# Kernel optimization log

Measured on AMD Instinct MI355X. Metric: run time of the kernel, lower is better.

Reference implementation:

```python
import jax, jax.numpy as jnp
import numpy as np
from jax import lax

B, T, V, E, H = 4096, 80, 10000, 100, 64


def setup_inputs() -> dict:
    key = jax.random.key(0)
    ks = jax.random.split(key, 8)
    return {
        "tokens": jax.random.randint(ks[0], (B, T), 0, V, dtype=jnp.int32),
        "emb": jax.random.normal(ks[1], (V, E), jnp.float32) * 0.05,
        "Wx0": jax.random.normal(ks[2], (E, H), jnp.float32) * (1.0 / np.sqrt(E)),
        "Wh0": jax.random.normal(ks[3], (H, H), jnp.float32) * (1.0 / np.sqrt(H)),
        "b0": jnp.zeros((H,), jnp.float32),
        "Wx1": jax.random.normal(ks[4], (H, H), jnp.float32) * (1.0 / np.sqrt(H)),
        "Wh1": jax.random.normal(ks[5], (H, H), jnp.float32) * (1.0 / np.sqrt(H)),
        "b1": jnp.zeros((H,), jnp.float32),
        "Wout": jax.random.normal(ks[6], (H, 1), jnp.float32) * (1.0 / np.sqrt(H)),
        "bout": jnp.zeros((1,), jnp.float32),
    }


def reference(tokens, emb, Wx0, Wh0, b0, Wx1, Wh1, b1, Wout, bout):
    # Embedding lookup: [B, T, E]
    x = emb[tokens]
    batch = x.shape[0]
    h0 = jnp.zeros((batch, Wh0.shape[0]), x.dtype)
    h1 = jnp.zeros((batch, Wh1.shape[0]), x.dtype)

    def step(carry, xt):
        h0, h1 = carry
        # SimpleRNNCell: h = tanh(x @ Wx + h_prev @ Wh + b)  (dropout off in eval)
        h0 = jnp.tanh(xt @ Wx0 + h0 @ Wh0 + b0)
        h1 = jnp.tanh(h0 @ Wx1 + h1 @ Wh1 + b1)
        return (h0, h1), None

    # scan over time: xs has shape [T, B, E]
    (h0, h1), _ = lax.scan(step, (h0, h1), jnp.swapaxes(x, 0, 1))
    logits = h1 @ Wout + bout  # [B, 1]
    return jax.nn.sigmoid(logits)
```

## Files before the change

### kernel.cpp

```cpp
#include <hip/hip_runtime.h>

#define BB 4096
#define TT 80
#define VV 10000
#define EE 100
#define HH 64
#define STR 68

typedef _Float16 f16x8 __attribute__((ext_vector_type(8)));
typedef _Float16 f16x4 __attribute__((ext_vector_type(4)));
typedef __attribute__((ext_vector_type(4))) float f4v;

#define MFMA(w, s, c) __builtin_amdgcn_mfma_f32_16x16x32_f16((w), (s), (c), 0, 0, 0)

#define BAR() do { asm volatile("s_waitcnt lgkmcnt(0)" ::: "memory"); \
                   __builtin_amdgcn_s_barrier();                      \
                   asm volatile("" ::: "memory"); } while (0)

__device__ __forceinline__ float fast_tanh(float x) {
    float e = __builtin_amdgcn_exp2f(x * 2.8853900817779268f);
    return 1.0f - 2.0f * __builtin_amdgcn_rcpf(e + 1.0f);
}

__device__ __forceinline__ void load_wfrag(const float* __restrict__ W, int kf, int g,
                                           int c, f16x8& hi, f16x8& lo) {
    union { _Float16 h[8]; f16x8 v; } th, tl;
#pragma unroll
    for (int i = 0; i < 8; ++i) {
        float wv = W[(32 * kf + 8 * g + i) * HH + c];
        _Float16 hf = (_Float16)wv;
        th.h[i] = hf;
        tl.h[i] = (_Float16)(wv - (float)hf);
    }
    hi = th.v;
    lo = tl.v;
}

__global__ __launch_bounds__(256) void emb2_kernel(const float* __restrict__ emb,
                                                   const float* __restrict__ Wx0,
                                                   const float* __restrict__ b0,
                                                   _Float16* __restrict__ emb2h) {
    const int tid = threadIdx.x;
    const int wid = tid >> 6;
    const int l = tid & 63;
    const int g = l >> 4;
    const int r16 = l & 15;
    const int c = 16 * wid + r16;
    const int jcol = 16 * wid + 4 * g;
    const int vr = blockIdx.x * 16 + r16;

    f16x8 wa[4];
#pragma unroll
    for (int kf = 0; kf < 4; ++kf) {
        union { _Float16 h[8]; f16x8 v; } t;
#pragma unroll
        for (int i = 0; i < 8; ++i) {
            int e = 32 * kf + 8 * g + i;
            t.h[i] = (e < EE) ? (_Float16)Wx0[e * HH + c] : (_Float16)0.f;
        }
        wa[kf] = t.v;
    }
    const float* er = emb + (size_t)vr * EE;
    f4v acc = *(const f4v*)&b0[jcol];
#pragma unroll
    for (int kf = 0; kf < 4; ++kf) {
        union { _Float16 h[8]; f16x8 v; } tb;
#pragma unroll
        for (int i = 0; i < 8; ++i) {
            int e = 32 * kf + 8 * g + i;
            tb.h[i] = (e < EE) ? (_Float16)er[e] : (_Float16)0.f;
        }
        acc = MFMA(wa[kf], tb.v, acc);
    }
    f16x4 o;
#pragma unroll
    for (int q = 0; q < 4; ++q) o[q] = (_Float16)acc[q];
    *(f16x4*)&emb2h[(size_t)vr * HH + jcol] = o;
}

__global__ __launch_bounds__(512, 1) void rnn_pipe(
    const int* __restrict__ tokens, const _Float16* __restrict__ emb2,
    const float* __restrict__ Wh0, const float* __restrict__ Wx1,
    const float* __restrict__ Wh1, const float* __restrict__ b1,
    const float* __restrict__ Wout, const float* __restrict__ bout,
    float* __restrict__ out) {
    __shared__ __align__(16) _Float16 H0[2][16][STR];
    __shared__ __align__(16) _Float16 H1[2][16][STR];
    __shared__ __align__(16) int tokT[TT][16];
    __shared__ float Pred[4][16];

    const int tid = threadIdx.x;
    const int w8 = tid >> 6;
    const int l = tid & 63;
    const int g = l >> 4;
    const int r16 = l & 15;
    const bool isL0 = (w8 < 4);
    const int tile = isL0 ? w8 : (w8 - 4);
    const int c = 16 * tile + r16;
    const int jcol = 16 * tile + 4 * g;
    const int R = blockIdx.x * 16;

    for (int i = tid; i < 16 * TT; i += 512) {
        int r = i / TT, t = i - r * TT;
        tokT[t][r] = tokens[R * TT + i] << 7;
    }

    f16x8 wAh[2], wAl[2], wBh[2], wBl[2];
    if (isL0) {
        load_wfrag(Wh0, 0, g, c, wAh[0], wAl[0]);
        load_wfrag(Wh0, 1, g, c, wAh[1], wAl[1]);
        wBh[0] = wBh[1] = wBl[0] = wBl[1] = (f16x8)0;
    } else {
        load_wfrag(Wx1, 0, g, c, wAh[0], wAl[0]);
        load_wfrag(Wx1, 1, g, c, wAh[1], wAl[1]);
        load_wfrag(Wh1, 0, g, c, wBh[0], wBl[0]);
        load_wfrag(Wh1, 1, g, c, wBh[1], wBl[1]);
    }
    const f4v b1v = *(const f4v*)&b1[jcol];
    const f4v wov = *(const f4v*)&Wout[jcol];
    const f4v z4 = {0.f, 0.f, 0.f, 0.f};
    const char* ebase = (const char*)emb2 + (size_t)jcol * 2;

    BAR();

    f16x8 a0[2] = {(f16x8)0, (f16x8)0};
    f16x8 a1[2] = {(f16x8)0, (f16x8)0};

    f16x4 xc = (f16x4)0, xn = (f16x4)0;
    if (isL0) {
        int tb0 = tokT[0][r16];
        int tb1 = tokT[1][r16];
        xc = *(const f16x4*)(ebase + tb0);
        xn = *(const f16x4*)(ebase + tb1);
        f16x4 ph;
#pragma unroll
        for (int q = 0; q < 4; ++q) ph[q] = (_Float16)fast_tanh((float)xc[q]);
        *(f16x4*)&H0[0][r16][jcol] = ph;
        xc = xn;
    }
    BAR();
    a0[0] = *(const f16x8*)&H0[0][r16][8 * g];
    a0[1] = *(const f16x8*)&H0[0][r16][32 + 8 * g];

#pragma unroll 2
    for (int p = 1; p <= TT - 1; ++p) {
        const int par = p & 1;
        if (isL0) {
            int pn = (p + 1 <= TT - 1) ? p + 1 : TT - 1;
            int tb = tokT[pn][r16];
            xn = *(const f16x4*)(ebase + tb);
            f4v A1 = {(float)xc[0], (float)xc[1], (float)xc[2], (float)xc[3]};
            A1 = MFMA(wAh[0], a0[0], A1);
            A1 = MFMA(wAh[1], a0[1], A1);
            f4v A2 = MFMA(wAl[0], a0[0], z4);
            A2 = MFMA(wAl[1], a0[1], A2);
            f4v acc0 = A1 + A2;
            f16x4 p0;
#pragma unroll
            for (int q = 0; q < 4; ++q) p0[q] = (_Float16)fast_tanh(acc0[q]);
            *(f16x4*)&H0[par][r16][jcol] = p0;
            xc = xn;
        } else {
            f4v C1 = b1v;
            C1 = MFMA(wAh[0], a0[0], C1);
            C1 = MFMA(wAh[1], a0[1], C1);
            f4v C2 = MFMA(wAl[0], a0[0], z4);
            C2 = MFMA(wAl[1], a0[1], C2);
            f4v C3 = MFMA(wBh[0], a1[0], z4);
            C3 = MFMA(wBh[1], a1[1], C3);
            f4v C4 = MFMA(wBl[0], a1[0], z4);
            C4 = MFMA(wBl[1], a1[1], C4);
            f4v acc1 = (C1 + C2) + (C3 + C4);
            f16x4 p1;
#pragma unroll
            for (int q = 0; q < 4; ++q) p1[q] = (_Float16)fast_tanh(acc1[q]);
            *(f16x4*)&H1[par][r16][jcol] = p1;
        }
        BAR();
        a0[0] = *(const f16x8*)&H0[par][r16][8 * g];
        a0[1] = *(const f16x8*)&H0[par][r16][32 + 8 * g];
        if (!isL0) {
            a1[0] = *(const f16x8*)&H1[par][r16][8 * g];
            a1[1] = *(const f16x8*)&H1[par][r16][32 + 8 * g];
        }
    }

    if (!isL0) {
        f4v C1 = b1v;
        C1 = MFMA(wAh[0], a0[0], C1);
        C1 = MFMA(wAh[1], a0[1], C1);
        f4v C2 = MFMA(wAl[0], a0[0], z4);
        C2 = MFMA(wAl[1], a0[1], C2);
        f4v C3 = MFMA(wBh[0], a1[0], z4);
        C3 = MFMA(wBh[1], a1[1], C3);
        f4v C4 = MFMA(wBl[0], a1[0], z4);
        C4 = MFMA(wBl[1], a1[1], C4);
        f4v acc1 = (C1 + C2) + (C3 + C4);
        float pp = fast_tanh(acc1[0]) * wov[0];
        pp = fmaf(fast_tanh(acc1[1]), wov[1], pp);
        pp = fmaf(fast_tanh(acc1[2]), wov[2], pp);
        pp = fmaf(fast_tanh(acc1[3]), wov[3], pp);
        pp += __shfl_xor(pp, 16, 64);
        pp += __shfl_xor(pp, 32, 64);
        if (l < 16) Pred[tile][l] = pp;
    }
    BAR();
    if (tid < 16) {
        float logit = Pred[0][tid] + Pred[1][tid] + Pred[2][tid] +
                      Pred[3][tid] + bout[0];
        out[R + tid] = __builtin_amdgcn_rcpf(
            1.0f + __builtin_amdgcn_exp2f(-1.4426950408889634f * logit));
    }
}

extern "C" void kernel_launch(void* const* d_in, const int* in_sizes, int n_in,
                              void* d_out, int out_size, void* d_ws, size_t ws_size,
                              hipStream_t stream) {
    const int*   tokens = (const int*)  d_in[0];
    const float* emb    = (const float*)d_in[1];
    const float* Wx0    = (const float*)d_in[2];
    const float* Wh0    = (const float*)d_in[3];
    const float* b0     = (const float*)d_in[4];
    const float* Wx1    = (const float*)d_in[5];
    const float* Wh1    = (const float*)d_in[6];
    const float* b1     = (const float*)d_in[7];
    const float* Wout   = (const float*)d_in[8];
    const float* bout   = (const float*)d_in[9];
    float* out  = (float*)d_out;
    _Float16* emb2h = (_Float16*)d_ws;

    emb2_kernel<<<VV / 16, 256, 0, stream>>>(emb, Wx0, b0, emb2h);
    rnn_pipe<<<BB / 16, 512, 0, stream>>>(tokens, emb2h, Wh0, Wx1, Wh1, b1,
                                          Wout, bout, out);
}
```

Baseline: 40.89 us.

## Split layer-1 RNN work into separate input and recurrent wave roles

Result: slower. 42.59 us (+4.2%).

```diff
diff --git a/kernel.cpp b/kernel.cpp
--- a/kernel.cpp
+++ b/kernel.cpp
@@ -6,6 +6,7 @@
 #define EE 100
 #define HH 64
 #define STR 68
+#define STRP 68
 
 typedef _Float16 f16x8 __attribute__((ext_vector_type(8)));
 typedef _Float16 f16x4 __attribute__((ext_vector_type(4)));
@@ -78,7 +79,7 @@
     *(f16x4*)&emb2h[(size_t)vr * HH + jcol] = o;
 }
 
-__global__ __launch_bounds__(512, 1) void rnn_pipe(
+__global__ __launch_bounds__(768, 1) void rnn_pipe(
     const int* __restrict__ tokens, const _Float16* __restrict__ emb2,
     const float* __restrict__ Wh0, const float* __restrict__ Wx1,
     const float* __restrict__ Wh1, const float* __restrict__ b1,
@@ -86,36 +87,30 @@
     float* __restrict__ out) {
     __shared__ __align__(16) _Float16 H0[2][16][STR];
     __shared__ __align__(16) _Float16 H1[2][16][STR];
+    __shared__ __align__(16) float PP[2][16][STRP];
     __shared__ __align__(16) int tokT[TT][16];
     __shared__ float Pred[4][16];
 
     const int tid = threadIdx.x;
-    const int w8 = tid >> 6;
+    const int w12 = tid >> 6;
     const int l = tid & 63;
     const int g = l >> 4;
     const int r16 = l & 15;
-    const bool isL0 = (w8 < 4);
-    const int tile = isL0 ? w8 : (w8 - 4);
+    const int role = w12 >> 2;
+    const int tile = w12 & 3;
     const int c = 16 * tile + r16;
     const int jcol = 16 * tile + 4 * g;
     const int R = blockIdx.x * 16;
 
-    for (int i = tid; i < 16 * TT; i += 512) {
+    for (int i = tid; i < 16 * TT; i += 768) {
         int r = i / TT, t = i - r * TT;
         tokT[t][r] = tokens[R * TT + i] << 7;
     }
 
-    f16x8 wAh[2], wAl[2], wBh[2], wBl[2];
-    if (isL0) {
-        load_wfrag(Wh0, 0, g, c, wAh[0], wAl[0]);
-        load_wfrag(Wh0, 1, g, c, wAh[1], wAl[1]);
-        wBh[0] = wBh[1] = wBl[0] = wBl[1] = (f16x8)0;
-    } else {
-        load_wfrag(Wx1, 0, g, c, wAh[0], wAl[0]);
-        load_wfrag(Wx1, 1, g, c, wAh[1], wAl[1]);
-        load_wfrag(Wh1, 0, g, c, wBh[0], wBl[0]);
-        load_wfrag(Wh1, 1, g, c, wBh[1], wBl[1]);
-    }
+    const float* Wsel = (role == 0) ? Wh0 : (role == 1 ? Wx1 : Wh1);
+    f16x8 wAh[2], wAl[2];
+    load_wfrag(Wsel, 0, g, c, wAh[0], wAl[0]);
+    load_wfrag(Wsel, 1, g, c, wAh[1], wAl[1]);
     const f4v b1v = *(const f4v*)&b1[jcol];
     const f4v wov = *(const f4v*)&Wout[jcol];
     const f4v z4 = {0.f, 0.f, 0.f, 0.f};
@@ -123,15 +118,12 @@
 
     BAR();
 
-    f16x8 a0[2] = {(f16x8)0, (f16x8)0};
-    f16x8 a1[2] = {(f16x8)0, (f16x8)0};
-
+    f16x8 as0 = (f16x8)0, as1 = (f16x8)0;
     f16x4 xc = (f16x4)0, xn = (f16x4)0;
-    if (isL0) {
-        int tb0 = tokT[0][r16];
-        int tb1 = tokT[1][r16];
-        xc = *(const f16x4*)(ebase + tb0);
-        xn = *(const f16x4*)(ebase + tb1);
+
+    if (role == 0) {
+        xc = *(const f16x4*)(ebase + tokT[0][r16]);
+        xn = *(const f16x4*)(ebase + tokT[1][r16]);
         f16x4 ph;
 #pragma unroll
         for (int q = 0; q < 4; ++q) ph[q] = (_Float16)fast_tanh((float)xc[q]);
@@ -139,67 +131,77 @@
         xc = xn;
     }
     BAR();
-    a0[0] = *(const f16x8*)&H0[0][r16][8 * g];
-    a0[1] = *(const f16x8*)&H0[0][r16][32 + 8 * g];
+    if (role != 2) {
+        as0 = *(const f16x8*)&H0[0][r16][8 * g];
+        as1 = *(const f16x8*)&H0[0][r16][32 + 8 * g];
+    }
 
 #pragma unroll 2
-    for (int p = 1; p <= TT - 1; ++p) {
-        const int par = p & 1;
-        if (isL0) {
-            int pn = (p + 1 <= TT - 1) ? p + 1 : TT - 1;
-            int tb = tokT[pn][r16];
-            xn = *(const f16x4*)(ebase + tb);
-            f4v A1 = {(float)xc[0], (float)xc[1], (float)xc[2], (float)xc[3]};
-            A1 = MFMA(wAh[0], a0[0], A1);
-            A1 = MFMA(wAh[1], a0[1], A1);
-            f4v A2 = MFMA(wAl[0], a0[0], z4);
-            A2 = MFMA(wAl[1], a0[1], A2);
-            f4v acc0 = A1 + A2;
-            f16x4 p0;
-#pragma unroll
-            for (int q = 0; q < 4; ++q) p0[q] = (_Float16)fast_tanh(acc0[q]);
-            *(f16x4*)&H0[par][r16][jcol] = p0;
-            xc = xn;
+    for (int q = 1; q <= 80; ++q) {
+        const int par = q & 1;
+        if (role == 0) {
+            if (q <= TT - 1) {
+                int pn = (q + 1 <= TT - 1) ? q + 1 : TT - 1;
+                xn = *(const f16x4*)(ebase + tokT[pn][r16]);
+                f4v C1 = {(float)xc[0], (float)xc[1], (float)xc[2], (float)xc[3]};
+                C1 = MFMA(wAh[0], as0, C1);
+                C1 = MFMA(wAh[1], as1, C1);
+                f4v C2 = MFMA(wAl[0], as0, z4);
+                C2 = MFMA(wAl[1], as1, C2);
+                f4v acc = C1 + C2;
+                f16x4 ph;
+#pragma unroll
+                for (int u = 0; u < 4; ++u) ph[u] = (_Float16)fast_tanh(acc[u]);
+                *(f16x4*)&H0[par][r16][jcol] = ph;
+                xc = xn;
+            }
+        } else if (role == 1) {
+            f4v C1 = b1v;
+            C1 = MFMA(wAh[0], as0, C1);
+            C1 = MFMA(wAh[1], as1, C1);
+            f4v C2 = MFMA(wAl[0], as0, z4);
+            C2 = MFMA(wAl[1], as1, C2);
+            f4v P = C1 + C2;
+            *(f4v*)&PP[par][r16][jcol] = P;
         } else {
-            f4v C1 = b1v;
-            C1 = MFMA(wAh[0], a0[0], C1);
-            C1 = MFMA(wAh[1], a0[1], C1);
-            f4v C2 = MFMA(wAl[0], a0[0], z4);
-            C2 = MFMA(wAl[1], a0[1], C2);
-            f4v C3 = MFMA(wBh[0], a1[0], z4);
-            C3 = MFMA(wBh[1], a1[1], C3);
-            f4v C4 = MFMA(wBl[0], a1[0], z4);
-            C4 = MFMA(wBl[1], a1[1], C4);
-            f4v acc1 = (C1 + C2) + (C3 + C4);
-            f16x4 p1;
-#pragma unroll
-            for (int q = 0; q < 4; ++q) p1[q] = (_Float16)fast_tanh(acc1[q]);
-            *(f16x4*)&H1[par][r16][jcol] = p1;
+            if (q >= 2) {
+                f4v C1 = *(const f4v*)&PP[par ^ 1][r16][jcol];
+                C1 = MFMA(wAh[0], as0, C1);
+                C1 = MFMA(wAh[1], as1, C1);
+                f4v C2 = MFMA(wAl[0], as0, z4);
+                C2 = MFMA(wAl[1], as1, C2);
+                f4v acc = C1 + C2;
+                f16x4 ph;
+#pragma unroll
+                for (int u = 0; u < 4; ++u) ph[u] = (_Float16)fast_tanh(acc[u]);
+                *(f16x4*)&H1[par][r16][jcol] = ph;
+            }
         }
         BAR();
-        a0[0] = *(const f16x8*)&H0[par][r16][8 * g];
-        a0[1] = *(const f16x8*)&H0[par][r16][32 + 8 * g];
-        if (!isL0) {
-            a1[0] = *(const f16x8*)&H1[par][r16][8 * g];
-            a1[1] = *(const f16x8*)&H1[par][r16][32 + 8 * g];
-        }
-    }
-
-    if (!isL0) {
-        f4v C1 = b1v;
-        C1 = MFMA(wAh[0], a0[0], C1);
-        C1 = MFMA(wAh[1], a0[1], C1);
-        f4v C2 = MFMA(wAl[0], a0[0], z4);
-        C2 = MFMA(wAl[1], a0[1], C2);
-        f4v C3 = MFMA(wBh[0], a1[0], z4);
-        C3 = MFMA(wBh[1], a1[1], C3);
-        f4v C4 = MFMA(wBl[0], a1[0], z4);
-        C4 = MFMA(wBl[1], a1[1], C4);
-        f4v acc1 = (C1 + C2) + (C3 + C4);
-        float pp = fast_tanh(acc1[0]) * wov[0];
-        pp = fmaf(fast_tanh(acc1[1]), wov[1], pp);
-        pp = fmaf(fast_tanh(acc1[2]), wov[2], pp);
-        pp = fmaf(fast_tanh(acc1[3]), wov[3], pp);
+        if (role != 2) {
+            if (q <= TT - 1) {
+                as0 = *(const f16x8*)&H0[par][r16][8 * g];
+                as1 = *(const f16x8*)&H0[par][r16][32 + 8 * g];
+            }
+        } else {
+            if (q >= 2) {
+                as0 = *(const f16x8*)&H1[par][r16][8 * g];
+                as1 = *(const f16x8*)&H1[par][r16][32 + 8 * g];
+            }
+        }
+    }
+
+    if (role == 2) {
+        f4v C1 = *(const f4v*)&PP[0][r16][jcol];
+        C1 = MFMA(wAh[0], as0, C1);
+        C1 = MFMA(wAh[1], as1, C1);
+        f4v C2 = MFMA(wAl[0], as0, z4);
+        C2 = MFMA(wAl[1], as1, C2);
+        f4v acc = C1 + C2;
+        float pp = fast_tanh(acc[0]) * wov[0];
+        pp = fmaf(fast_tanh(acc[1]), wov[1], pp);
+        pp = fmaf(fast_tanh(acc[2]), wov[2], pp);
+        pp = fmaf(fast_tanh(acc[3]), wov[3], pp);
         pp += __shfl_xor(pp, 16, 64);
         pp += __shfl_xor(pp, 32, 64);
         if (l < 16) Pred[tile][l] = pp;
@@ -230,6 +232,6 @@
     _Float16* emb2h = (_Float16*)d_ws;
 
     emb2_kernel<<<VV / 16, 256, 0, stream>>>(emb, Wx0, b0, emb2h);
-    rnn_pipe<<<BB / 16, 512, 0, stream>>>(tokens, emb2h, Wh0, Wx1, Wh1, b1,
+    rnn_pipe<<<BB / 16, 768, 0, stream>>>(tokens, emb2h, Wh0, Wx1, Wh1, b1,
                                           Wout, bout, out);
 }
```

## Move layer-1 input projection onto layer-0 waves via shared-memory handoff

Applied to the files above, without the earlier changes.

Result: slower. 54.02 us (+32.1%).

```diff
diff --git a/kernel.cpp b/kernel.cpp
--- a/kernel.cpp
+++ b/kernel.cpp
@@ -6,6 +6,7 @@
 #define EE 100
 #define HH 64
 #define STR 68
+#define STRP 68
 
 typedef _Float16 f16x8 __attribute__((ext_vector_type(8)));
 typedef _Float16 f16x4 __attribute__((ext_vector_type(4)));
@@ -86,6 +87,7 @@
     float* __restrict__ out) {
     __shared__ __align__(16) _Float16 H0[2][16][STR];
     __shared__ __align__(16) _Float16 H1[2][16][STR];
+    __shared__ __align__(16) float PP[2][16][STRP];
     __shared__ __align__(16) int tokT[TT][16];
     __shared__ float Pred[4][16];
 
@@ -109,12 +111,12 @@
     if (isL0) {
         load_wfrag(Wh0, 0, g, c, wAh[0], wAl[0]);
         load_wfrag(Wh0, 1, g, c, wAh[1], wAl[1]);
+        load_wfrag(Wx1, 0, g, c, wBh[0], wBl[0]);
+        load_wfrag(Wx1, 1, g, c, wBh[1], wBl[1]);
+    } else {
+        load_wfrag(Wh1, 0, g, c, wAh[0], wAl[0]);
+        load_wfrag(Wh1, 1, g, c, wAh[1], wAl[1]);
         wBh[0] = wBh[1] = wBl[0] = wBl[1] = (f16x8)0;
-    } else {
-        load_wfrag(Wx1, 0, g, c, wAh[0], wAl[0]);
-        load_wfrag(Wx1, 1, g, c, wAh[1], wAl[1]);
-        load_wfrag(Wh1, 0, g, c, wBh[0], wBl[0]);
-        load_wfrag(Wh1, 1, g, c, wBh[1], wBl[1]);
     }
     const f4v b1v = *(const f4v*)&b1[jcol];
     const f4v wov = *(const f4v*)&Wout[jcol];
@@ -124,14 +126,12 @@
     BAR();
 
     f16x8 a0[2] = {(f16x8)0, (f16x8)0};
-    f16x8 a1[2] = {(f16x8)0, (f16x8)0};
-
+    f4v Pin = z4;
     f16x4 xc = (f16x4)0, xn = (f16x4)0;
+
     if (isL0) {
-        int tb0 = tokT[0][r16];
-        int tb1 = tokT[1][r16];
-        xc = *(const f16x4*)(ebase + tb0);
-        xn = *(const f16x4*)(ebase + tb1);
+        xc = *(const f16x4*)(ebase + tokT[0][r16]);
+        xn = *(const f16x4*)(ebase + tokT[1][r16]);
         f16x4 ph;
 #pragma unroll
         for (int q = 0; q < 4; ++q) ph[q] = (_Float16)fast_tanh((float)xc[q]);
@@ -139,63 +139,72 @@
         xc = xn;
     }
     BAR();
-    a0[0] = *(const f16x8*)&H0[0][r16][8 * g];
-    a0[1] = *(const f16x8*)&H0[0][r16][32 + 8 * g];
+    if (isL0) {
+        a0[0] = *(const f16x8*)&H0[0][r16][8 * g];
+        a0[1] = *(const f16x8*)&H0[0][r16][32 + 8 * g];
+    }
 
 #pragma unroll 2
-    for (int p = 1; p <= TT - 1; ++p) {
+    for (int p = 1; p <= 80; ++p) {
         const int par = p & 1;
         if (isL0) {
-            int pn = (p + 1 <= TT - 1) ? p + 1 : TT - 1;
-            int tb = tokT[pn][r16];
-            xn = *(const f16x4*)(ebase + tb);
-            f4v A1 = {(float)xc[0], (float)xc[1], (float)xc[2], (float)xc[3]};
-            A1 = MFMA(wAh[0], a0[0], A1);
-            A1 = MFMA(wAh[1], a0[1], A1);
-            f4v A2 = MFMA(wAl[0], a0[0], z4);
-            A2 = MFMA(wAl[1], a0[1], A2);
-            f4v acc0 = A1 + A2;
-            f16x4 p0;
-#pragma unroll
-            for (int q = 0; q < 4; ++q) p0[q] = (_Float16)fast_tanh(acc0[q]);
-            *(f16x4*)&H0[par][r16][jcol] = p0;
-            xc = xn;
+            if (p <= TT - 1) {
+                if (p <= TT - 2)
+                    xn = *(const f16x4*)(ebase + tokT[p + 1][r16]);
+                f4v A1 = {(float)xc[0], (float)xc[1], (float)xc[2], (float)xc[3]};
+                A1 = MFMA(wAh[0], a0[0], A1);
+                A1 = MFMA(wAh[1], a0[1], A1);
+                f4v A2 = MFMA(wAl[0], a0[0], z4);
+                A2 = MFMA(wAl[1], a0[1], A2);
+                f4v acc0 = A1 + A2;
+                f16x4 p0;
+#pragma unroll
+                for (int q = 0; q < 4; ++q) p0[q] = (_Float16)fast_tanh(acc0[q]);
+                *(f16x4*)&H0[par][r16][jcol] = p0;
+                xc = xn;
+            }
+            f4v C1 = b1v;
+            C1 = MFMA(wBh[0], a0[0], C1);
+            C1 = MFMA(wBh[1], a0[1], C1);
+            f4v C2 = MFMA(wBl[0], a0[0], z4);
+            C2 = MFMA(wBl[1], a0[1], C2);
+            *(f4v*)&PP[par][r16][jcol] = C1 + C2;
         } else {
-            f4v C1 = b1v;
-            C1 = MFMA(wAh[0], a0[0], C1);
-            C1 = MFMA(wAh[1], a0[1], C1);
-            f4v C2 = MFMA(wAl[0], a0[0], z4);
-            C2 = MFMA(wAl[1], a0[1], C2);
-            f4v C3 = MFMA(wBh[0], a1[0], z4);
-            C3 = MFMA(wBh[1], a1[1], C3);
-            f4v C4 = MFMA(wBl[0], a1[0], z4);
-            C4 = MFMA(wBl[1], a1[1], C4);
-            f4v acc1 = (C1 + C2) + (C3 + C4);
-            f16x4 p1;
-#pragma unroll
-            for (int q = 0; q < 4; ++q) p1[q] = (_Float16)fast_tanh(acc1[q]);
-            *(f16x4*)&H1[par][r16][jcol] = p1;
+            if (p >= 2) {
+                f4v C1 = Pin;
+                C1 = MFMA(wAh[0], a0[0], C1);
+                C1 = MFMA(wAh[1], a0[1], C1);
+                f4v C2 = MFMA(wAl[0], a0[0], z4);
+                C2 = MFMA(wAl[1], a0[1], C2);
+                f4v acc1 = C1 + C2;
+                f16x4 p1;
+#pragma unroll
+                for (int q = 0; q < 4; ++q) p1[q] = (_Float16)fast_tanh(acc1[q]);
+                *(f16x4*)&H1[par][r16][jcol] = p1;
+            }
         }
         BAR();
-        a0[0] = *(const f16x8*)&H0[par][r16][8 * g];
-        a0[1] = *(const f16x8*)&H0[par][r16][32 + 8 * g];
-        if (!isL0) {
-            a1[0] = *(const f16x8*)&H1[par][r16][8 * g];
-            a1[1] = *(const f16x8*)&H1[par][r16][32 + 8 * g];
+        if (isL0) {
+            if (p <= TT - 1) {
+                a0[0] = *(const f16x8*)&H0[par][r16][8 * g];
+                a0[1] = *(const f16x8*)&H0[par][r16][32 + 8 * g];
+            }
+        } else {
+            if (p >= 2) {
+                a0[0] = *(const f16x8*)&H1[par][r16][8 * g];
+                a0[1] = *(const f16x8*)&H1[par][r16][32 + 8 * g];
+            }
+            Pin = *(const f4v*)&PP[par][r16][jcol];
         }
     }
 
     if (!isL0) {
-        f4v C1 = b1v;
+        f4v C1 = Pin;
         C1 = MFMA(wAh[0], a0[0], C1);
         C1 = MFMA(wAh[1], a0[1], C1);
         f4v C2 = MFMA(wAl[0], a0[0], z4);
         C2 = MFMA(wAl[1], a0[1], C2);
-        f4v C3 = MFMA(wBh[0], a1[0], z4);
-        C3 = MFMA(wBh[1], a1[1], C3);
-        f4v C4 = MFMA(wBl[0], a1[0], z4);
-        C4 = MFMA(wBl[1], a1[1], C4);
-        f4v acc1 = (C1 + C2) + (C3 + C4);
+        f4v acc1 = C1 + C2;
         float pp = fast_tanh(acc1[0]) * wov[0];
         pp = fmaf(fast_tanh(acc1[1]), wov[1], pp);
         pp = fmaf(fast_tanh(acc1[2]), wov[2], pp);
```
